# Performance work log

Measured on AMD Instinct MI355X. Metric: run time of the kernel, lower is better.

## Reference

```python
import jax, jax.numpy as jnp
import numpy as np

TAU = 0.2  # world.kgc_temp
EPS = 1e-12  # F.normalize eps


def _l2_normalize(z):
    n = jnp.linalg.norm(z, axis=1, keepdims=True)
    return z / jnp.maximum(n, EPS)


def setup_inputs() -> dict:
    key = jax.random.key(0)
    k1, k2 = jax.random.split(key)
    N, D = 8192, 512
    z1 = jax.random.normal(k1, (N, D), dtype=jnp.float32)
    z2 = jax.random.normal(k2, (N, D), dtype=jnp.float32)
    return {"z1": z1, "z2": z2}


def _semi_loss(h1, h2):
    # h1, h2: [N, D] already L2-normalized
    refl_sim = jnp.exp(jnp.matmul(h1, h1.T) / TAU)      # [N, N]
    between_sim = jnp.exp(jnp.matmul(h1, h2.T) / TAU)   # [N, N]
    denom = refl_sim.sum(axis=1) + between_sim.sum(axis=1) - jnp.diag(refl_sim)
    return -jnp.log(jnp.diag(between_sim) / denom)      # [N]


def reference(z1, z2):
    h1 = _l2_normalize(z1)
    h2 = _l2_normalize(z2)
    l1 = _semi_loss(h1, h2)
    l2 = _semi_loss(h2, h1)
    return jnp.sum((l1 + l2) * 0.5)
```

## Files before the change

### kernel.cpp

```cpp
#include <hip/hip_runtime.h>
#include <hip/hip_bf16.h>
#include <math.h>
#include <stdint.h>

#define N_ROWS 8192
#define DIM 512
#define INV_TAU 5.0f
#define EXP5 148.41315910257660342f

typedef float f32x4 __attribute__((ext_vector_type(4)));
typedef int   i32x4 __attribute__((ext_vector_type(4)));
typedef int   i32x8 __attribute__((ext_vector_type(8)));

union Frag8 {
  i32x8 v8;
  struct { i32x4 lo, hi; } s;
};

__device__ __forceinline__ void gload_lds16(const void* g, void* l) {
  __builtin_amdgcn_global_load_lds(
      (__attribute__((address_space(1))) void*)(void*)g,
      (__attribute__((address_space(3))) void*)l,
      16, 0, 0);
}

__global__ __launch_bounds__(256) void normalize_kernel(
    const float* __restrict__ z1, const float* __restrict__ z2,
    uint8_t* __restrict__ h1p, uint8_t* __restrict__ h2p,
    float* __restrict__ dvec,
    float* __restrict__ r1, float* __restrict__ r2,
    float* __restrict__ brow, float* __restrict__ bcol,
    float* __restrict__ out) {
  __shared__ __align__(16) uint8_t L[16384];
  const int t = threadIdx.x;
  const int lr = t >> 4;
  const int kb = t & 15;
  const int row = blockIdx.x * 16 + lr;
  const float4* p1 = (const float4*)(z1 + (size_t)row * DIM + kb * 32);
  const float4* p2 = (const float4*)(z2 + (size_t)row * DIM + kb * 32);
  float4 a[8], b[8];
  float s1 = 0.f, s2 = 0.f, s3 = 0.f;
#pragma unroll
  for (int i = 0; i < 8; i++) {
    a[i] = p1[i]; b[i] = p2[i];
    s1 += a[i].x*a[i].x + a[i].y*a[i].y + a[i].z*a[i].z + a[i].w*a[i].w;
    s2 += b[i].x*b[i].x + b[i].y*b[i].y + b[i].z*b[i].z + b[i].w*b[i].w;
    s3 += a[i].x*b[i].x + a[i].y*b[i].y + a[i].z*b[i].z + a[i].w*b[i].w;
  }
  for (int m = 1; m <= 8; m <<= 1) {
    s1 += __shfl_xor(s1, m);
    s2 += __shfl_xor(s2, m);
    s3 += __shfl_xor(s3, m);
  }
  const float inv1 = 1.0f / fmaxf(sqrtf(s1), 1e-12f);
  const float inv2 = 1.0f / fmaxf(sqrtf(s2), 1e-12f);
  int w1[8], w2[8];
#pragma unroll
  for (int i = 0; i < 8; i++) {
    int w = __builtin_amdgcn_cvt_pk_fp8_f32(a[i].x*inv1, a[i].y*inv1, 0, false);
    w1[i] = __builtin_amdgcn_cvt_pk_fp8_f32(a[i].z*inv1, a[i].w*inv1, w, true);
    w = __builtin_amdgcn_cvt_pk_fp8_f32(b[i].x*inv2, b[i].y*inv2, 0, false);
    w2[i] = __builtin_amdgcn_cvt_pk_fp8_f32(b[i].z*inv2, b[i].w*inv2, w, true);
  }
  const int ks = kb >> 2;
  const int l = (kb & 3) * 16 + lr;
  *(int4*)(L + ks * 2048 + l * 16)          = make_int4(w1[0], w1[1], w1[2], w1[3]);
  *(int4*)(L + ks * 2048 + 1024 + l * 16)   = make_int4(w1[4], w1[5], w1[6], w1[7]);
  *(int4*)(L + 8192 + ks * 2048 + l * 16)        = make_int4(w2[0], w2[1], w2[2], w2[3]);
  *(int4*)(L + 8192 + ks * 2048 + 1024 + l * 16) = make_int4(w2[4], w2[5], w2[6], w2[7]);
  if (kb == 0) dvec[row] = s3 * inv1 * inv2;
  if (t < 16) {
    const int i = blockIdx.x * 16 + t;
    r1[i] = 0.f; r2[i] = 0.f; brow[i] = 0.f; bcol[i] = 0.f;
    if (i == 0) out[0] = 0.f;
  }
  __syncthreads();
  const size_t gb = (size_t)blockIdx.x * 8192;
  int4* g1 = (int4*)(h1p + gb);
  int4* g2 = (int4*)(h2p + gb);
  const int4* Lv = (const int4*)L;
  g1[t]       = Lv[t];
  g1[t + 256] = Lv[t + 256];
  g2[t]       = Lv[t + 512];
  g2[t + 256] = Lv[t + 768];
}

__global__ __launch_bounds__(256, 3) void expsum_kernel(
    const uint8_t* __restrict__ h1p, const uint8_t* __restrict__ h2p,
    float* __restrict__ r1, float* __restrict__ r2,
    float* __restrict__ brow, float* __restrict__ bcol) {
  __shared__ __align__(16) uint8_t Bs[49152];

  const int u = (blockIdx.x & 7) * 1032 + (blockIdx.x >> 3);
  int bj = (int)((sqrt(8.0 * (double)u + 1.0) - 1.0) * 0.5);
  if (bj * (bj + 1) / 2 > u) bj--;
  if ((bj + 1) * (bj + 2) / 2 <= u) bj++;
  const int bi = u - bj * (bj + 1) / 2;
  const bool diagb = (bi == bj);

  const uint8_t* Ap = (bi < 64) ? h1p : h2p;
  const uint8_t* Bp = (bj < 64) ? h1p : h2p;
  float* rowsOut = (bi < 64) ? ((bj < 64) ? r1 : brow) : r2;
  float* colsOut = (bj < 64) ? r1 : ((bi < 64) ? bcol : r2);
  const int iOutBase = (bi & 63) * 128;
  const int jOutBase = (bj & 63) * 128;

  const int t = threadIdx.x;
  const int w = t >> 6;
  const int lane = t & 63;
  const int l16 = lane & 15;
  const int kq = lane >> 4;

  const uint8_t* Bgp = Bp + (size_t)(bj & 63) * 65536;

#define STAGE(KS, BUFOFS)                                                   \
  do {                                                                      \
    _Pragma("unroll") for (int r_ = 0; r_ < 4; r_++) {                      \
      const int cb_ = (r_ * 256 + t) * 16;                                  \
      gload_lds16(Bgp + ((cb_ >> 11) << 13) + (KS)*2048 + (cb_ & 2047),     \
                  Bs + (BUFOFS) + cb_);                                     \
    }                                                                       \
  } while (0)

#define COMPUTE_CHUNK(KS, BUFOFS)                                           \
  do {                                                                      \
    const uint8_t* Bc_ = (const uint8_t*)Bs + (BUFOFS) + lane * 16;         \
    _Pragma("unroll") for (int fn_ = 0; fn_ < 8; fn_++) {                   \
      Frag8 B0_;                                                            \
      B0_.s.lo = *(const i32x4*)(Bc_ + fn_ * 2048);                         \
      B0_.s.hi = *(const i32x4*)(Bc_ + fn_ * 2048 + 1024);                  \
      _Pragma("unroll") for (int fm_ = 0; fm_ < 2; fm_++)                   \
        acc[fm_][fn_] = __builtin_amdgcn_mfma_scale_f32_16x16x128_f8f6f4(   \
            Af[fm_][KS].v8, B0_.v8, acc[fm_][fn_],                          \
            0, 0, 0, 0x7F7F7F7F, 0, 0x7F7F7F7F);                            \
    }                                                                       \
  } while (0)

  STAGE(0, 0);
  STAGE(1, 16384);

  const uint8_t* Ag =
      Ap + ((size_t)((bi & 63) * 8 + w * 2)) * 8192 + (size_t)lane * 16 + 4096;
  Frag8 Af[2][4];
#pragma unroll
  for (int f = 0; f < 2; f++)
#pragma unroll
    for (int ks = 0; ks < 4; ks++) {
      const int ofs = f * 8192 + ks * 2048 - 4096;
      Af[f][ks].s.lo = *(const i32x4*)(Ag + ofs);
      Af[f][ks].s.hi = *(const i32x4*)(Ag + ofs + 1024);
    }

  f32x4 acc[2][8];
#pragma unroll
  for (int a = 0; a < 2; a++)
#pragma unroll
    for (int b = 0; b < 8; b++)
#pragma unroll
      for (int r = 0; r < 4; r++) acc[a][b][r] = 0.0f;


  asm volatile("s_waitcnt vmcnt(4)" ::: "memory");
  __builtin_amdgcn_s_barrier();
  __builtin_amdgcn_sched_barrier(0);
  STAGE(2, 32768);
  __builtin_amdgcn_s_setprio(1);
  COMPUTE_CHUNK(0, 0);
  __builtin_amdgcn_s_setprio(0);

  asm volatile("s_waitcnt vmcnt(4)" ::: "memory");
  __builtin_amdgcn_s_barrier();
  __builtin_amdgcn_sched_barrier(0);
  STAGE(3, 0);
  __builtin_amdgcn_s_setprio(1);
  COMPUTE_CHUNK(1, 16384);
  __builtin_amdgcn_s_setprio(0);

  asm volatile("s_waitcnt vmcnt(4)" ::: "memory");
  __builtin_amdgcn_s_barrier();
  __builtin_amdgcn_sched_barrier(0);
  __builtin_amdgcn_s_setprio(1);
  COMPUTE_CHUNK(2, 32768);
  __builtin_amdgcn_s_setprio(0);

  asm volatile("s_waitcnt vmcnt(0)" ::: "memory");
  __builtin_amdgcn_s_barrier();
  __builtin_amdgcn_sched_barrier(0);
  __builtin_amdgcn_s_setprio(1);
  COMPUTE_CHUNK(3, 0);
  __builtin_amdgcn_s_setprio(0);

#undef STAGE
#undef COMPUTE_CHUNK

  float rowp[2][4];
  float colp[8];
#pragma unroll
  for (int fm = 0; fm < 2; fm++)
#pragma unroll
    for (int r = 0; r < 4; r++) rowp[fm][r] = 0.0f;
#pragma unroll
  for (int fn = 0; fn < 8; fn++) colp[fn] = 0.0f;

  if (!diagb) {
#pragma unroll
    for (int fm = 0; fm < 2; fm++)
#pragma unroll
      for (int fn = 0; fn < 8; fn++)
#pragma unroll
        for (int r = 0; r < 4; r++) {
          const float e = __expf(acc[fm][fn][r] * INV_TAU);
          rowp[fm][r] += e;
          colp[fn] += e;
        }
  } else {
#pragma unroll
    for (int fm = 0; fm < 2; fm++)
#pragma unroll
      for (int fn = 0; fn < 8; fn++)
#pragma unroll
        for (int r = 0; r < 4; r++) {
          const int ti = w * 32 + fm * 16 + kq * 4 + r;
          const int tj = fn * 16 + l16;
          const float e = __expf(acc[fm][fn][r] * INV_TAU);
          rowp[fm][r] += (ti <= tj) ? e : 0.0f;
          colp[fn] += (ti < tj) ? e : 0.0f;
        }
  }

  __syncthreads();
  float* lds_col = (float*)Bs;
  float* lds_row = lds_col + 128;
  if (t < 128) lds_col[t] = 0.0f;
  __syncthreads();

#pragma unroll
  for (int fm = 0; fm < 2; fm++) {
#pragma unroll
    for (int r = 0; r < 4; r++) {
      float v = rowp[fm][r];
      v += __shfl_xor(v, 1);
      v += __shfl_xor(v, 2);
      v += __shfl_xor(v, 4);
      v += __shfl_xor(v, 8);
      if (l16 == 0) lds_row[w * 32 + fm * 16 + kq * 4 + r] = v;
    }
  }
#pragma unroll
  for (int fn = 0; fn < 8; fn++) {
    float v = colp[fn];
    v += __shfl_xor(v, 16);
    v += __shfl_xor(v, 32);
    if (kq == 0) atomicAdd(&lds_col[fn * 16 + l16], v);
  }
  __syncthreads();

  if (t < 128) atomicAdd(&rowsOut[iOutBase + t], lds_row[t]);
  else         atomicAdd(&colsOut[jOutBase + (t - 128)], lds_col[t - 128]);
}

__global__ __launch_bounds__(256) void finalize_kernel(
    const float* __restrict__ r1, const float* __restrict__ r2,
    const float* __restrict__ brow, const float* __restrict__ bcol,
    const float* __restrict__ dvec, float* __restrict__ out) {
  const int i = blockIdx.x * 256 + threadIdx.x;
  const float den1 = r1[i] + brow[i] - EXP5;
  const float den2 = r2[i] + bcol[i] - EXP5;
  float v = 0.5f * (logf(den1) + logf(den2)) - INV_TAU * dvec[i];
  for (int m = 32; m; m >>= 1) v += __shfl_xor(v, m);
  __shared__ float red[4];
  const int wave = threadIdx.x >> 6;
  if ((threadIdx.x & 63) == 0) red[wave] = v;
  __syncthreads();
  if (threadIdx.x == 0) atomicAdd(out, red[0] + red[1] + red[2] + red[3]);
}

extern "C" void kernel_launch(void* const* d_in, const int* in_sizes, int n_in,
                              void* d_out, int out_size, void* d_ws, size_t ws_size,
                              hipStream_t stream) {
  const float* z1 = (const float*)d_in[0];
  const float* z2 = (const float*)d_in[1];
  float* out = (float*)d_out;

  char* ws = (char*)d_ws;
  uint8_t* h1p = (uint8_t*)ws;
  uint8_t* h2p = (uint8_t*)(ws + (4u << 20));
  float* r1   = (float*)(ws + (8u << 20));
  float* r2   = r1 + N_ROWS;
  float* brow = r2 + N_ROWS;
  float* bcol = brow + N_ROWS;
  float* dvec = bcol + N_ROWS;

  normalize_kernel<<<N_ROWS / 16, 256, 0, stream>>>(
      z1, z2, h1p, h2p, dvec, r1, r2, brow, bcol, out);
  expsum_kernel<<<8256, 256, 0, stream>>>(h1p, h2p, r1, r2, brow, bcol);
  finalize_kernel<<<N_ROWS / 256, 256, 0, stream>>>(r1, r2, brow, bcol, dvec, out);
}
```

Before: 182.5 us.

## Process up to four column tiles per block with resident A fragments

Result: slower. 545.3 us (+198.8%).

```diff
diff --git a/kernel.cpp b/kernel.cpp
--- a/kernel.cpp
+++ b/kernel.cpp
@@ -86,38 +86,31 @@
 }
 
 __global__ __launch_bounds__(256, 3) void expsum_kernel(
-    const uint8_t* __restrict__ h1p, const uint8_t* __restrict__ h2p,
+    const uint8_t* __restrict__ Wp,
     float* __restrict__ r1, float* __restrict__ r2,
     float* __restrict__ brow, float* __restrict__ bcol) {
   __shared__ __align__(16) uint8_t Bs[49152];
-
-  const int u = (blockIdx.x & 7) * 1032 + (blockIdx.x >> 3);
-  int bj = (int)((sqrt(8.0 * (double)u + 1.0) - 1.0) * 0.5);
-  if (bj * (bj + 1) / 2 > u) bj--;
-  if ((bj + 1) * (bj + 2) / 2 <= u) bj++;
-  const int bi = u - bj * (bj + 1) / 2;
-  const bool diagb = (bi == bj);
-
-  const uint8_t* Ap = (bi < 64) ? h1p : h2p;
-  const uint8_t* Bp = (bj < 64) ? h1p : h2p;
-  float* rowsOut = (bi < 64) ? ((bj < 64) ? r1 : brow) : r2;
-  float* colsOut = (bj < 64) ? r1 : ((bi < 64) ? bcol : r2);
-  const int iOutBase = (bi & 63) * 128;
-  const int jOutBase = (bj & 63) * 128;
+  __shared__ __align__(16) float Red[256];
+
+  const int bi  = blockIdx.x;
+  const int bj0 = bi + 4 * (int)blockIdx.y;
+  if (bj0 > 127) return;
+  const int L = (128 - bj0 < 4) ? (128 - bj0) : 4;
 
   const int t = threadIdx.x;
   const int w = t >> 6;
   const int lane = t & 63;
   const int l16 = lane & 15;
   const int kq = lane >> 4;
-
-  const uint8_t* Bgp = Bp + (size_t)(bj & 63) * 65536;
-
-#define STAGE(KS, BUFOFS)                                                   \
+  const int iOutBase = (bi & 63) * 128;
+
+  const uint8_t* Bg0 = Wp + (size_t)bj0 * 65536;
+
+#define STAGE(BGP, KS, BUFOFS)                                              \
   do {                                                                      \
     _Pragma("unroll") for (int r_ = 0; r_ < 4; r_++) {                      \
       const int cb_ = (r_ * 256 + t) * 16;                                  \
-      gload_lds16(Bgp + ((cb_ >> 11) << 13) + (KS)*2048 + (cb_ & 2047),     \
+      gload_lds16((BGP) + ((cb_ >> 11) << 13) + (KS)*2048 + (cb_ & 2047),   \
                   Bs + (BUFOFS) + cb_);                                     \
     }                                                                       \
   } while (0)
@@ -136,11 +129,16 @@
     }                                                                       \
   } while (0)
 
-  STAGE(0, 0);
-  STAGE(1, 16384);
+#define VMW(N) asm volatile("s_waitcnt vmcnt(" #N ")" ::: "memory")
+#define LGK0   asm volatile("s_waitcnt lgkmcnt(0)" ::: "memory")
+#define BAR    __builtin_amdgcn_s_barrier()
+#define SCH    __builtin_amdgcn_sched_barrier(0)
+
+  STAGE(Bg0, 0, 0);
+  STAGE(Bg0, 1, 16384);
 
   const uint8_t* Ag =
-      Ap + ((size_t)((bi & 63) * 8 + w * 2)) * 8192 + (size_t)lane * 16 + 4096;
+      Wp + (size_t)(bi * 8 + w * 2) * 8192 + (size_t)lane * 16 + 4096;
   Frag8 Af[2][4];
 #pragma unroll
   for (int f = 0; f < 2; f++)
@@ -159,104 +157,131 @@
 #pragma unroll
       for (int r = 0; r < 4; r++) acc[a][b][r] = 0.0f;
 
-
-  asm volatile("s_waitcnt vmcnt(4)" ::: "memory");
-  __builtin_amdgcn_s_barrier();
-  __builtin_amdgcn_sched_barrier(0);
-  STAGE(2, 32768);
-  __builtin_amdgcn_s_setprio(1);
-  COMPUTE_CHUNK(0, 0);
-  __builtin_amdgcn_s_setprio(0);
-
-  asm volatile("s_waitcnt vmcnt(4)" ::: "memory");
-  __builtin_amdgcn_s_barrier();
-  __builtin_amdgcn_sched_barrier(0);
-  STAGE(3, 0);
-  __builtin_amdgcn_s_setprio(1);
-  COMPUTE_CHUNK(1, 16384);
-  __builtin_amdgcn_s_setprio(0);
-
-  asm volatile("s_waitcnt vmcnt(4)" ::: "memory");
-  __builtin_amdgcn_s_barrier();
-  __builtin_amdgcn_sched_barrier(0);
-  __builtin_amdgcn_s_setprio(1);
-  COMPUTE_CHUNK(2, 32768);
-  __builtin_amdgcn_s_setprio(0);
-
-  asm volatile("s_waitcnt vmcnt(0)" ::: "memory");
-  __builtin_amdgcn_s_barrier();
-  __builtin_amdgcn_sched_barrier(0);
-  __builtin_amdgcn_s_setprio(1);
-  COMPUTE_CHUNK(3, 0);
-  __builtin_amdgcn_s_setprio(0);
+  float rowp[2][4];
+#pragma unroll
+  for (int fm = 0; fm < 2; fm++)
+#pragma unroll
+    for (int r = 0; r < 4; r++) rowp[fm][r] = 0.0f;
+
+  int b0 = 0, b1 = 16384, b2 = 32768;
+
+  for (int tt = 0; tt < L; ++tt) {
+    const int bj = bj0 + tt;
+    const bool haveNext = (tt + 1 < L);
+    const uint8_t* Bg  = Bg0 + (size_t)tt * 65536;
+    const uint8_t* Bgn = Bg + 65536;
+
+    VMW(4); BAR; SCH;
+    STAGE(Bg, 2, b2);
+    __builtin_amdgcn_s_setprio(1);
+    COMPUTE_CHUNK(0, b0);
+    __builtin_amdgcn_s_setprio(0);
+
+    VMW(4); BAR; SCH;
+    STAGE(Bg, 3, b0);
+    __builtin_amdgcn_s_setprio(1);
+    COMPUTE_CHUNK(1, b1);
+    __builtin_amdgcn_s_setprio(0);
+
+    VMW(4); BAR; SCH;
+    if (haveNext) STAGE(Bgn, 0, b1);
+    __builtin_amdgcn_s_setprio(1);
+    COMPUTE_CHUNK(2, b2);
+    __builtin_amdgcn_s_setprio(0);
+
+    if (haveNext) { VMW(4); } else { VMW(0); }
+    BAR; SCH;
+    if (haveNext) STAGE(Bgn, 1, b2);
+    __builtin_amdgcn_s_setprio(1);
+    COMPUTE_CHUNK(3, b0);
+    __builtin_amdgcn_s_setprio(0);
+
+    { const int n0 = b1, n1 = b2, n2 = b0; b0 = n0; b1 = n1; b2 = n2; }
+
+    const bool diagb = (bj == bi);
+    const bool flushR = (!haveNext) || (bi < 64 && bj == 63);
+    float* rowsOut = (bi < 64) ? ((bj < 64) ? r1 : brow) : r2;
+    float* colsOut = (bj < 64) ? r1 : ((bi < 64) ? bcol : r2);
+    const int jOutBase = (bj & 63) * 128;
+
+    float colp[8];
+#pragma unroll
+    for (int fn = 0; fn < 8; fn++) colp[fn] = 0.0f;
+
+    if (!diagb) {
+#pragma unroll
+      for (int fm = 0; fm < 2; fm++)
+#pragma unroll
+        for (int fn = 0; fn < 8; fn++)
+#pragma unroll
+          for (int r = 0; r < 4; r++) {
+            const float e = __expf(acc[fm][fn][r] * INV_TAU);
+            rowp[fm][r] += e;
+            colp[fn] += e;
+          }
+    } else {
+#pragma unroll
+      for (int fm = 0; fm < 2; fm++)
+#pragma unroll
+        for (int fn = 0; fn < 8; fn++)
+#pragma unroll
+          for (int r = 0; r < 4; r++) {
+            const int ti = w * 32 + fm * 16 + kq * 4 + r;
+            const int tj = fn * 16 + l16;
+            const float e = __expf(acc[fm][fn][r] * INV_TAU);
+            rowp[fm][r] += (ti <= tj) ? e : 0.0f;
+            colp[fn] += (ti < tj) ? e : 0.0f;
+          }
+    }
+#pragma unroll
+    for (int fm = 0; fm < 2; fm++)
+#pragma unroll
+      for (int fn = 0; fn < 8; fn++)
+#pragma unroll
+        for (int r = 0; r < 4; r++) acc[fm][fn][r] = 0.0f;
+
+    if (t < 128) Red[128 + t] = 0.0f;
+    LGK0; BAR; SCH;
+#pragma unroll
+    for (int fn = 0; fn < 8; fn++) {
+      float v = colp[fn];
+      v += __shfl_xor(v, 16);
+      v += __shfl_xor(v, 32);
+      if (kq == 0) atomicAdd(&Red[128 + fn * 16 + l16], v);
+    }
+    if (flushR) {
+#pragma unroll
+      for (int fm = 0; fm < 2; fm++)
+#pragma unroll
+        for (int r = 0; r < 4; r++) {
+          float v = rowp[fm][r];
+          v += __shfl_xor(v, 1);
+          v += __shfl_xor(v, 2);
+          v += __shfl_xor(v, 4);
+          v += __shfl_xor(v, 8);
+          if (l16 == 0) Red[w * 32 + fm * 16 + kq * 4 + r] = v;
+        }
+    }
+    LGK0; BAR; SCH;
+    if (t < 128) {
+      if (flushR) atomicAdd(&rowsOut[iOutBase + t], Red[t]);
+    } else {
+      atomicAdd(&colsOut[jOutBase + (t - 128)], Red[t]);
+    }
+    if (flushR) {
+#pragma unroll
+      for (int fm = 0; fm < 2; fm++)
+#pragma unroll
+        for (int r = 0; r < 4; r++) rowp[fm][r] = 0.0f;
+    }
+  }
 
 #undef STAGE
 #undef COMPUTE_CHUNK
-
-  float rowp[2][4];
-  float colp[8];
-#pragma unroll
-  for (int fm = 0; fm < 2; fm++)
-#pragma unroll
-    for (int r = 0; r < 4; r++) rowp[fm][r] = 0.0f;
-#pragma unroll
-  for (int fn = 0; fn < 8; fn++) colp[fn] = 0.0f;
-
-  if (!diagb) {
-#pragma unroll
-    for (int fm = 0; fm < 2; fm++)
-#pragma unroll
-      for (int fn = 0; fn < 8; fn++)
-#pragma unroll
-        for (int r = 0; r < 4; r++) {
-          const float e = __expf(acc[fm][fn][r] * INV_TAU);
-          rowp[fm][r] += e;
-          colp[fn] += e;
-        }
-  } else {
-#pragma unroll
-    for (int fm = 0; fm < 2; fm++)
-#pragma unroll
-      for (int fn = 0; fn < 8; fn++)
-#pragma unroll
-        for (int r = 0; r < 4; r++) {
-          const int ti = w * 32 + fm * 16 + kq * 4 + r;
-          const int tj = fn * 16 + l16;
-          const float e = __expf(acc[fm][fn][r] * INV_TAU);
-          rowp[fm][r] += (ti <= tj) ? e : 0.0f;
-          colp[fn] += (ti < tj) ? e : 0.0f;
-        }
-  }
-
-  __syncthreads();
-  float* lds_col = (float*)Bs;
-  float* lds_row = lds_col + 128;
-  if (t < 128) lds_col[t] = 0.0f;
-  __syncthreads();
-
-#pragma unroll
-  for (int fm = 0; fm < 2; fm++) {
-#pragma unroll
-    for (int r = 0; r < 4; r++) {
-      float v = rowp[fm][r];
-      v += __shfl_xor(v, 1);
-      v += __shfl_xor(v, 2);
-      v += __shfl_xor(v, 4);
-      v += __shfl_xor(v, 8);
-      if (l16 == 0) lds_row[w * 32 + fm * 16 + kq * 4 + r] = v;
-    }
-  }
-#pragma unroll
-  for (int fn = 0; fn < 8; fn++) {
-    float v = colp[fn];
-    v += __shfl_xor(v, 16);
-    v += __shfl_xor(v, 32);
-    if (kq == 0) atomicAdd(&lds_col[fn * 16 + l16], v);
-  }
-  __syncthreads();
-
-  if (t < 128) atomicAdd(&rowsOut[iOutBase + t], lds_row[t]);
-  else         atomicAdd(&colsOut[jOutBase + (t - 128)], lds_col[t - 128]);
+#undef VMW
+#undef LGK0
+#undef BAR
+#undef SCH
 }
 
 __global__ __launch_bounds__(256) void finalize_kernel(
@@ -293,6 +318,6 @@
 
   normalize_kernel<<<N_ROWS / 16, 256, 0, stream>>>(
       z1, z2, h1p, h2p, dvec, r1, r2, brow, bcol, out);
-  expsum_kernel<<<8256, 256, 0, stream>>>(h1p, h2p, r1, r2, brow, bcol);
+  expsum_kernel<<<dim3(128, 32), 256, 0, stream>>>(h1p, r1, r2, brow, bcol);
   finalize_kernel<<<N_ROWS / 256, 256, 0, stream>>>(r1, r2, brow, bcol, dvec, out);
 }
```
